# Kernel optimization log

Measured on AMD Instinct MI355X. Metric: run time of the kernel, lower is better.

## Reference

```python
import jax, jax.numpy as jnp
import numpy as np

N = 4096
IN_F = 256
H = 4
D = 64
WIN = 128
HALF = WIN // 2
TAU = 0.5
TOP_K = 32


def setup_inputs() -> dict:
    key = jax.random.key(0)
    ks = jax.random.split(key, 5)
    node_features = jax.random.normal(ks[0], (N, IN_F), dtype=jnp.float32)
    s = 1.0 / np.sqrt(IN_F)
    Wq = jax.random.normal(ks[1], (IN_F, H * D), dtype=jnp.float32) * s
    bq = jax.random.normal(ks[2], (H * D,), dtype=jnp.float32) * 0.01
    Wk = jax.random.normal(ks[3], (IN_F, H * D), dtype=jnp.float32) * s
    bk = jax.random.normal(ks[4], (H * D,), dtype=jnp.float32) * 0.01
    num_nodes_per_graph = jnp.full((8,), 512, dtype=jnp.int32)  # 8 graphs x 512 = N
    return {"node_features": node_features, "Wq": Wq, "bq": bq, "Wk": Wk,
            "bk": bk, "num_nodes_per_graph": num_nodes_per_graph, "num_relation": 1}


def reference(node_features, Wq, bq, Wk, bk, num_nodes_per_graph, num_relation):
    n = node_features.shape[0]
    scale = jnp.sqrt(jnp.asarray(D, node_features.dtype))

    Q = (node_features @ Wq + bq).reshape(n, H, D)
    K = (node_features @ Wk + bk).reshape(n, H, D)

    # segment boundaries (graph.num_nodes.repeat(num_relation) -> cumsum -> searchsorted)
    segment = jnp.tile(num_nodes_per_graph, num_relation)
    cum = jnp.cumsum(segment)
    i = jnp.arange(n)
    pos = jnp.searchsorted(cum, i, side='right')
    seg_start = jnp.where(pos == 0, 0, cum[jnp.maximum(pos - 1, 0)])
    seg_end = cum[jnp.minimum(pos, cum.shape[0] - 1)]

    start = jnp.maximum(seg_start, i - HALF)  # [N]
    end = jnp.minimum(seg_end, i + HALF)      # [N]

    gather_idx = start[:, None] + jnp.arange(WIN)[None, :]
    valid = gather_idx < end[:, None]
    gi = jnp.clip(gather_idx, 0, n - 1)
    Kw = jnp.where(valid[:, :, None, None], K[gi], 0.0)

    # scores over full window incl. zero padding (faithful: original does not mask softmax)
    scores = jnp.einsum('nhd,nmhd->nhm', Q, Kw) / scale / TAU
    attn = jax.nn.softmax(scores, axis=-1).mean(axis=1)

    # scatter attention rows into dense N x N (padded slots add 0)
    output = jnp.zeros((n, n), node_features.dtype).at[i[:, None], gi].add(
        jnp.where(valid, attn, 0.0))

    # gumbel_softmax_top_k(output, tau, hard=self.k) -> hard=True (k truthy)
    g = jax.random.gumbel(jax.random.key(42), output.shape, output.dtype)
    y_soft = jax.nn.softmax((output + g) / TAU, axis=-1)
    topk_idx = jax.lax.top_k(output, TOP_K)[1]                  # [N, TOP_K]
    y_hard = jnp.zeros_like(output).at[i[:, None], topk_idx].set(1.0)
    y = jax.lax.stop_gradient(y_hard - y_soft) + y_soft
    return y
```

## Files before the change

### kernel.cpp

```cpp
#include <hip/hip_runtime.h>

#define NF    256
#define HD    256
#define NH    4
#define DH    64
#define WINS  128
#define HALFW 64
#define TOPK  32
#define GROWS 32

typedef float vfloat4 __attribute__((ext_vector_type(4)));

__device__ __forceinline__ float dpp_add16(float v) {
    int x;
    x = __builtin_amdgcn_update_dpp(0, __float_as_int(v), 0xB1, 0xF, 0xF, true);
    v += __int_as_float(x);
    x = __builtin_amdgcn_update_dpp(0, __float_as_int(v), 0x4E, 0xF, 0xF, true);
    v += __int_as_float(x);
    x = __builtin_amdgcn_update_dpp(0, __float_as_int(v), 0x124, 0xF, 0xF, true);
    v += __int_as_float(x);
    x = __builtin_amdgcn_update_dpp(0, __float_as_int(v), 0x128, 0xF, 0xF, true);
    v += __int_as_float(x);
    return v;
}

__global__ __launch_bounds__(256, 2) void qk_gemm_kernel(
    const float* __restrict__ X,
    const float* __restrict__ Wq, const float* __restrict__ bq,
    const float* __restrict__ Wk, const float* __restrict__ bk,
    float* __restrict__ Qb, float* __restrict__ Kb, int n)
{
    const int t    = threadIdx.x;
    const int wave = t >> 6;
    const int lane = t & 63;
    const bool isK = (blockIdx.y != 0);
    const int half = blockIdx.z;
    const float* W   = isK ? Wk : Wq;
    const float* bia = isK ? bk : bq;
    float*       Out = isK ? Kb : Qb;

    const int gx = gridDim.x;
    int bswz = blockIdx.x;
    if ((gx & 7) == 0) {
        int chunk = gx >> 3;
        bswz = (blockIdx.x & 7) * chunk + (blockIdx.x >> 3);
    }
    const int r0  = bswz * GROWS + wave * 8;
    const int r0s = __builtin_amdgcn_readfirstlane(r0);
    const float* Xs = X + (size_t)r0s * NF;

    const int c0 = half * 128 + 2 * lane;

    float2 acc[8];
#pragma unroll
    for (int r = 0; r < 8; ++r) acc[r] = make_float2(0.f, 0.f);

    float2 wA[8], wB[8];
    const float* Wl = W + c0;

#pragma unroll
    for (int u = 0; u < 8; ++u)
        wA[u] = *(const float2*)(Wl + (size_t)u * HD);

    for (int k = 0; k < NF; k += 16) {
        if (k + 8 < NF) {
#pragma unroll
            for (int u = 0; u < 8; ++u)
                wB[u] = *(const float2*)(Wl + (size_t)(k + 8 + u) * HD);
        }
#pragma unroll
        for (int u = 0; u < 8; ++u) {
#pragma unroll
            for (int r = 0; r < 8; ++r) {
                float xk = Xs[r * NF + k + u];
                acc[r].x += xk * wA[u].x;
                acc[r].y += xk * wA[u].y;
            }
        }
        if (k + 16 < NF) {
#pragma unroll
            for (int u = 0; u < 8; ++u)
                wA[u] = *(const float2*)(Wl + (size_t)(k + 16 + u) * HD);
        }
#pragma unroll
        for (int u = 0; u < 8; ++u) {
#pragma unroll
            for (int r = 0; r < 8; ++r) {
                float xk = Xs[r * NF + k + 8 + u];
                acc[r].x += xk * wB[u].x;
                acc[r].y += xk * wB[u].y;
            }
        }
    }

    const float2 bv = *(const float2*)(bia + c0);
#pragma unroll
    for (int r = 0; r < 8; ++r) {
        acc[r].x += bv.x; acc[r].y += bv.y;
        *(float2*)(Out + (size_t)(r0 + r) * HD + c0) = acc[r];
    }
}

__global__ __launch_bounds__(256) void attn_topk_kernel(
    const float* __restrict__ Q,
    const float* __restrict__ K,
    const int* __restrict__ nnpg, int n_graphs,
    const int* __restrict__ nrel,
    float* __restrict__ out, int n)
{
    const int t    = threadIdx.x;
    const int wave = t >> 6;
    const int lane = t & 63;

    int i = blockIdx.x;
    const int nb = gridDim.x;
    if ((nb & 7) == 0) {
        int chunk = nb >> 3;
        i = (blockIdx.x & 7) * chunk + (blockIdx.x >> 3);
    }

    __shared__ float sc[NH][WINS + 8];
    __shared__ float pr[NH][WINS];
    __shared__ float attnv[WINS];
    __shared__ float slotval[WINS];

    int R = nrel[0];
    int total = n_graphs * R;
    int seg_start = 0, seg_end = n;
    int cum = 0;
    for (int e = 0; e < total; ++e) {
        int sz = nnpg[e % n_graphs];
        int nc = cum + sz;
        if (i < nc) { seg_start = cum; seg_end = nc; break; }
        cum = nc;
    }
    const int start = max(seg_start, i - HALFW);
    const int end   = min(seg_end,   i + HALFW);
    const int win   = end - start;

    const float4 q4 = *(const float4*)(Q + (size_t)i * HD + lane * 4);

#pragma unroll 8
    for (int j = 0; j < 32; ++j) {
        int row = wave + 4 * j;
        float v = 0.f;
        if (row < win) {
            float4 k4 = *(const float4*)(K + (size_t)(start + row) * HD + lane * 4);
            v = q4.x * k4.x + q4.y * k4.y + q4.z * k4.z + q4.w * k4.w;
        }
        v = dpp_add16(v);
        if ((lane & 15) == 0)
            sc[lane >> 4][row] = v * 0.25f;
    }

    vfloat4* orow = (vfloat4*)(out + (size_t)i * n);
    const int n4  = n >> 2;
    const int lo4 = start >> 2;
    const int hi4 = (end - 1) >> 2;
    const vfloat4 z4 = {0.f, 0.f, 0.f, 0.f};
    for (int c4 = t; c4 < n4; c4 += 256) {
        if (c4 >= lo4 && c4 <= hi4) continue;
        __builtin_nontemporal_store(z4, &orow[c4]);
    }
    __syncthreads();

    {
        float v0 = sc[wave][lane], v1 = sc[wave][lane + 64];
        float mx = fmaxf(v0, v1);
#pragma unroll
        for (int off = 32; off > 0; off >>= 1) mx = fmaxf(mx, __shfl_xor(mx, off));
        float e0 = expf(v0 - mx), e1 = expf(v1 - mx);
        float sm = e0 + e1;
#pragma unroll
        for (int off = 32; off > 0; off >>= 1) sm += __shfl_xor(sm, off);
        pr[wave][lane]      = e0 / sm;
        pr[wave][lane + 64] = e1 / sm;
    }
    __syncthreads();

    if (t < WINS) {
        float a = 0.25f * (pr[0][t] + pr[1][t] + pr[2][t] + pr[3][t]);
        attnv[t] = (t < win) ? a : -1.0f;
    }
    __syncthreads();

    if (t < WINS) {
        float v = attnv[t];
        int cnt = 0;
#pragma unroll
        for (int j4 = 0; j4 < WINS / 4; ++j4) {
            float4 a4 = *(const float4*)&attnv[j4 * 4];
            int jb = j4 * 4;
            cnt += (a4.x > v) || (a4.x == v && (jb + 0) < t);
            cnt += (a4.y > v) || (a4.y == v && (jb + 1) < t);
            cnt += (a4.z > v) || (a4.z == v && (jb + 2) < t);
            cnt += (a4.w > v) || (a4.w == v && (jb + 3) < t);
        }
        slotval[t] = (t < win && cnt < TOPK) ? 1.0f : 0.0f;
    }
    __syncthreads();

    {
        int c4 = lo4 + t;
        if (c4 <= hi4) {
            int c = c4 << 2;
            int o0 = c - start, o1 = o0 + 1, o2 = o0 + 2, o3 = o0 + 3;
            vfloat4 v4;
            v4.x = (o0 >= 0 && o0 < WINS) ? slotval[o0] : 0.f;
            v4.y = (o1 >= 0 && o1 < WINS) ? slotval[o1] : 0.f;
            v4.z = (o2 >= 0 && o2 < WINS) ? slotval[o2] : 0.f;
            v4.w = (o3 >= 0 && o3 < WINS) ? slotval[o3] : 0.f;
            __builtin_nontemporal_store(v4, &orow[c4]);
        }
    }
}

extern "C" void kernel_launch(void* const* d_in, const int* in_sizes, int n_in,
                              void* d_out, int out_size, void* d_ws, size_t ws_size,
                              hipStream_t stream)
{
    const float* X  = (const float*)d_in[0];
    const float* Wq = (const float*)d_in[1];
    const float* bq = (const float*)d_in[2];
    const float* Wk = (const float*)d_in[3];
    const float* bk = (const float*)d_in[4];
    const int* nnpg = (const int*)d_in[5];
    const int* nrel = (const int*)d_in[6];

    const int n = in_sizes[0] / NF;
    const int n_graphs = in_sizes[5];

    float* Qb = (float*)d_ws;
    float* Kb = Qb + (size_t)n * HD;
    float* out = (float*)d_out;

    dim3 gg(n / GROWS, 2, 2);
    qk_gemm_kernel<<<gg, 256, 0, stream>>>(X, Wq, bq, Wk, bk, Qb, Kb, n);

    attn_topk_kernel<<<n, 256, 0, stream>>>(Qb, Kb, nnpg, n_graphs, nrel, out, n);
}
```

Before: 135.3 us.

## Process four query rows per block to share windowed K loads

The attention/top-k kernel now handles four consecutive query nodes per block. It loads each K row in the union of their windows once and computes dot products against all four queries, so K traffic and block count drop by about four. Softmax, averaging and rank selection are batched over the four rows. The 4096-wide row zeroing is unchanged and likely dominates, so the gain depends on how much K reading mattered. The result also relies on n being divisible by four.

```diff
diff --git a/kernel.cpp b/kernel.cpp
--- a/kernel.cpp
+++ b/kernel.cpp
@@ -8,6 +8,7 @@
 #define HALFW 64
 #define TOPK  32
 #define GROWS 32
+#define NPB   4
 
 typedef float vfloat4 __attribute__((ext_vector_type(4)));
 
@@ -112,60 +113,83 @@
     const int wave = t >> 6;
     const int lane = t & 63;
 
-    int i = blockIdx.x;
+    int b = blockIdx.x;
     const int nb = gridDim.x;
     if ((nb & 7) == 0) {
         int chunk = nb >> 3;
-        i = (blockIdx.x & 7) * chunk + (blockIdx.x >> 3);
-    }
-
-    __shared__ float sc[NH][WINS + 8];
-    __shared__ float pr[NH][WINS];
-    __shared__ float attnv[WINS];
-    __shared__ float slotval[WINS];
-
-    int R = nrel[0];
-    int total = n_graphs * R;
-    int seg_start = 0, seg_end = n;
-    int cum = 0;
-    for (int e = 0; e < total; ++e) {
-        int sz = nnpg[e % n_graphs];
-        int nc = cum + sz;
-        if (i < nc) { seg_start = cum; seg_end = nc; break; }
-        cum = nc;
-    }
-    const int start = max(seg_start, i - HALFW);
-    const int end   = min(seg_end,   i + HALFW);
-    const int win   = end - start;
-
-    const float4 q4 = *(const float4*)(Q + (size_t)i * HD + lane * 4);
-
-#pragma unroll 8
-    for (int j = 0; j < 32; ++j) {
-        int row = wave + 4 * j;
-        float v = 0.f;
-        if (row < win) {
-            float4 k4 = *(const float4*)(K + (size_t)(start + row) * HD + lane * 4);
-            v = q4.x * k4.x + q4.y * k4.y + q4.z * k4.z + q4.w * k4.w;
-        }
-        v = dpp_add16(v);
-        if ((lane & 15) == 0)
-            sc[lane >> 4][row] = v * 0.25f;
-    }
-
-    vfloat4* orow = (vfloat4*)(out + (size_t)i * n);
-    const int n4  = n >> 2;
-    const int lo4 = start >> 2;
-    const int hi4 = (end - 1) >> 2;
+        b = (blockIdx.x & 7) * chunk + (blockIdx.x >> 3);
+    }
+    const int i0 = b * NPB;
+
+    __shared__ float sc[NH][NPB][WINS];
+    __shared__ float attnv[NPB][WINS];
+    __shared__ float slotval[NPB][WINS];
+
+    const int R = nrel[0];
+    const int total = n_graphs * R;
+    int startv[NPB], endv[NPB];
+#pragma unroll
+    for (int nn = 0; nn < NPB; ++nn) {
+        const int i = i0 + nn;
+        int cs = 0, s0 = 0, e0 = n;
+        for (int e = 0; e < total; ++e) {
+            int sz = nnpg[e % n_graphs];
+            int nc = cs + sz;
+            if (i < nc) { s0 = cs; e0 = nc; break; }
+            cs = nc;
+        }
+        startv[nn] = max(s0, i - HALFW);
+        endv[nn]   = min(e0, i + HALFW);
+    }
+    const int u0    = startv[0];
+    const int urows = endv[NPB - 1] - u0;
+
+    {
+        float4* scv = (float4*)&sc[0][0][0];
+        for (int idx = t; idx < NH * NPB * WINS / 4; idx += 256)
+            scv[idx] = make_float4(0.f, 0.f, 0.f, 0.f);
+    }
+
+    float4 q4[NPB];
+#pragma unroll
+    for (int nn = 0; nn < NPB; ++nn)
+        q4[nn] = *(const float4*)(Q + (size_t)(i0 + nn) * HD + lane * 4);
+
+    __syncthreads();
+
+#pragma unroll 4
+    for (int r = wave; r < urows; r += 4) {
+        const int row = u0 + r;
+        const float4 k4 = *(const float4*)(K + (size_t)row * HD + lane * 4);
+#pragma unroll
+        for (int nn = 0; nn < NPB; ++nn) {
+            float v = q4[nn].x * k4.x + q4[nn].y * k4.y
+                    + q4[nn].z * k4.z + q4[nn].w * k4.w;
+            v = dpp_add16(v);
+            const int rel = row - startv[nn];
+            if ((lane & 15) == 0 &&
+                (unsigned)rel < (unsigned)(endv[nn] - startv[nn]))
+                sc[lane >> 4][nn][rel] = v * 0.25f;
+        }
+    }
+
+    const int n4 = n >> 2;
     const vfloat4 z4 = {0.f, 0.f, 0.f, 0.f};
-    for (int c4 = t; c4 < n4; c4 += 256) {
-        if (c4 >= lo4 && c4 <= hi4) continue;
-        __builtin_nontemporal_store(z4, &orow[c4]);
-    }
-    __syncthreads();
-
-    {
-        float v0 = sc[wave][lane], v1 = sc[wave][lane + 64];
+#pragma unroll
+    for (int nn = 0; nn < NPB; ++nn) {
+        vfloat4* orow = (vfloat4*)(out + (size_t)(i0 + nn) * n);
+        const int lo4 = startv[nn] >> 2;
+        const int hi4 = (endv[nn] - 1) >> 2;
+        for (int c4 = t; c4 < n4; c4 += 256) {
+            if (c4 >= lo4 && c4 <= hi4) continue;
+            __builtin_nontemporal_store(z4, &orow[c4]);
+        }
+    }
+    __syncthreads();
+
+#pragma unroll
+    for (int nn = 0; nn < NPB; ++nn) {
+        float v0 = sc[wave][nn][lane], v1 = sc[wave][nn][lane + 64];
         float mx = fmaxf(v0, v1);
 #pragma unroll
         for (int off = 32; off > 0; off >>= 1) mx = fmaxf(mx, __shfl_xor(mx, off));
@@ -173,43 +197,56 @@
         float sm = e0 + e1;
 #pragma unroll
         for (int off = 32; off > 0; off >>= 1) sm += __shfl_xor(sm, off);
-        pr[wave][lane]      = e0 / sm;
-        pr[wave][lane + 64] = e1 / sm;
-    }
-    __syncthreads();
-
-    if (t < WINS) {
-        float a = 0.25f * (pr[0][t] + pr[1][t] + pr[2][t] + pr[3][t]);
-        attnv[t] = (t < win) ? a : -1.0f;
-    }
-    __syncthreads();
-
-    if (t < WINS) {
-        float v = attnv[t];
+        sc[wave][nn][lane]      = e0 / sm;
+        sc[wave][nn][lane + 64] = e1 / sm;
+    }
+    __syncthreads();
+
+#pragma unroll
+    for (int hh = 0; hh < 2; ++hh) {
+        const int idx = t + hh * 256;
+        const int nn = idx >> 7, s = idx & 127;
+        float a = 0.25f * (sc[0][nn][s] + sc[1][nn][s]
+                         + sc[2][nn][s] + sc[3][nn][s]);
+        attnv[nn][s] = (s < endv[nn] - startv[nn]) ? a : -1.0f;
+    }
+    __syncthreads();
+
+#pragma unroll
+    for (int hh = 0; hh < 2; ++hh) {
+        const int idx = t + hh * 256;
+        const int nn = idx >> 7, s = idx & 127;
+        const float v = attnv[nn][s];
         int cnt = 0;
 #pragma unroll
         for (int j4 = 0; j4 < WINS / 4; ++j4) {
-            float4 a4 = *(const float4*)&attnv[j4 * 4];
+            float4 a4 = *(const float4*)&attnv[nn][j4 * 4];
             int jb = j4 * 4;
-            cnt += (a4.x > v) || (a4.x == v && (jb + 0) < t);
-            cnt += (a4.y > v) || (a4.y == v && (jb + 1) < t);
-            cnt += (a4.z > v) || (a4.z == v && (jb + 2) < t);
-            cnt += (a4.w > v) || (a4.w == v && (jb + 3) < t);
-        }
-        slotval[t] = (t < win && cnt < TOPK) ? 1.0f : 0.0f;
+            cnt += (a4.x > v) || (a4.x == v && (jb + 0) < s);
+            cnt += (a4.y > v) || (a4.y == v && (jb + 1) < s);
+            cnt += (a4.z > v) || (a4.z == v && (jb + 2) < s);
+            cnt += (a4.w > v) || (a4.w == v && (jb + 3) < s);
+        }
+        slotval[nn][s] =
+            (s < endv[nn] - startv[nn] && cnt < TOPK) ? 1.0f : 0.0f;
     }
     __syncthreads();
 
     {
-        int c4 = lo4 + t;
+        const int nn = wave;
+        vfloat4* orow = (vfloat4*)(out + (size_t)(i0 + nn) * n);
+        const int st = startv[nn];
+        const int lo4 = st >> 2;
+        const int hi4 = (endv[nn] - 1) >> 2;
+        const int c4 = lo4 + lane;
         if (c4 <= hi4) {
-            int c = c4 << 2;
-            int o0 = c - start, o1 = o0 + 1, o2 = o0 + 2, o3 = o0 + 3;
+            const int c = c4 << 2;
+            const int o0 = c - st, o1 = o0 + 1, o2 = o0 + 2, o3 = o0 + 3;
             vfloat4 v4;
-            v4.x = (o0 >= 0 && o0 < WINS) ? slotval[o0] : 0.f;
-            v4.y = (o1 >= 0 && o1 < WINS) ? slotval[o1] : 0.f;
-            v4.z = (o2 >= 0 && o2 < WINS) ? slotval[o2] : 0.f;
-            v4.w = (o3 >= 0 && o3 < WINS) ? slotval[o3] : 0.f;
+            v4.x = (o0 >= 0 && o0 < WINS) ? slotval[nn][o0] : 0.f;
+            v4.y = (o1 >= 0 && o1 < WINS) ? slotval[nn][o1] : 0.f;
+            v4.z = (o2 >= 0 && o2 < WINS) ? slotval[nn][o2] : 0.f;
+            v4.w = (o3 >= 0 && o3 < WINS) ? slotval[nn][o3] : 0.f;
             __builtin_nontemporal_store(v4, &orow[c4]);
         }
     }
@@ -237,5 +274,6 @@
     dim3 gg(n / GROWS, 2, 2);
     qk_gemm_kernel<<<gg, 256, 0, stream>>>(X, Wq, bq, Wk, bk, Qb, Kb, n);
 
-    attn_topk_kernel<<<n, 256, 0, stream>>>(Qb, Kb, nnpg, n_graphs, nrel, out, n);
-}
+    attn_topk_kernel<<<n / NPB, 256, 0, stream>>>(Qb, Kb, nnpg, n_graphs, nrel,
+                                                  out, n);
+}
```

New measurement: 136.7 us (median of 2 runs). No clear change (+1.1%).
